# Kernel optimization log

Hardware: AMD Instinct MI355X
Metric: run time of the kernel (lower is better)

Reference implementation:

```python
import math
import jax, jax.numpy as jnp
from jax import lax
import numpy as np

NUM_POINTS = 256      # K sampled points
HIDDEN_DIM = 768
NUM_FREQS = 10
INPUT_DIM = 3 * 2 * NUM_FREQS  # 60


def _fps_indices(pts, k):
    """Furthest point sampling indices for a single cloud pts: [N,3] -> [k] int32.
    Standard iterative FPS starting from index 0."""
    n = pts.shape[0]
    idxs0 = jnp.zeros((k,), dtype=jnp.int32)
    dists0 = jnp.full((n,), jnp.inf, dtype=pts.dtype)

    def body(i, state):
        idxs, dists = state
        last = pts[idxs[i - 1]]                       # [3]
        d = jnp.sum((pts - last) ** 2, axis=-1)       # [N]
        dists = jnp.minimum(dists, d)
        idxs = idxs.at[i].set(jnp.argmax(dists).astype(jnp.int32))
        return (idxs, dists)

    idxs, _ = lax.fori_loop(1, k, body, (idxs0, dists0))
    return idxs


def setup_inputs() -> dict:
    key = jax.random.key(0)
    k1, k2, k3 = jax.random.split(key, 3)
    B, N = 32, 262144
    point_cloud = jax.random.normal(k1, (B, N, 3), dtype=jnp.float32)
    # Xavier-uniform Linear weight [out, in], zero bias (matches _init_weights)
    limit = math.sqrt(6.0 / (INPUT_DIM + HIDDEN_DIM))
    W = jax.random.uniform(k2, (HIDDEN_DIM, INPUT_DIM), jnp.float32, -limit, limit)
    b = jnp.zeros((HIDDEN_DIM,), dtype=jnp.float32)
    return {"point_cloud": point_cloud, "W": W, "b": b}


def reference(point_cloud, W, b):
    B = point_cloud.shape[0]
    # sanitize non-finite (matches torch.where(isfinite, x, 0))
    pc = jnp.where(jnp.isfinite(point_cloud), point_cloud, 0.0)

    # --- furthest point sampling (indices are non-differentiable) ---
    idxs = jax.vmap(lambda p: _fps_indices(lax.stop_gradient(p), NUM_POINTS))(pc)  # [B,K]
    sampled = jnp.take_along_axis(pc, idxs[:, :, None], axis=1)  # [B,K,3]

    # --- per-sample normalization: center then scale by max bbox dim ---
    centroid = jnp.mean(sampled, axis=1, keepdims=True)           # [B,1,3]
    centered = sampled - centroid                                  # [B,K,3]
    bbox = jnp.max(centered, axis=1) - jnp.min(centered, axis=1)   # [B,3]
    max_dim = jnp.max(bbox, axis=-1)                               # [B]
    scale = jnp.where(max_dim > 1e-8, max_dim, 1.0)
    normed = centered / scale[:, None, None]                       # [B,K,3]

    # --- Fourier encoding: sin/cos of coords * 2^f * pi ---
    freqs = jnp.power(2.0, jnp.arange(NUM_FREQS, dtype=jnp.float32))  # [F]
    scaled = normed[..., None] * freqs * jnp.float32(math.pi)         # [B,K,3,F]
    enc = jnp.stack([jnp.sin(scaled), jnp.cos(scaled)], axis=-1)      # [B,K,3,F,2]
    enc = enc.reshape(B, NUM_POINTS, INPUT_DIM)                       # [B,K,60]

    # --- linear projection (torch Linear: x @ W.T + b) ---
    return jnp.einsum('bkd,hd->bkh', enc, W) + b                      # [B,K,768]
```

## Files before the change

### kernel.cpp

```cpp
#include <hip/hip_runtime.h>

#define BATCH 32
#define NPTS  262144
#define KSAMP 256
#define NF    10
#define INDIM 60
#define HID   768

#define NBLK_PER_B 8
#define SLICE (NPTS/NBLK_PER_B)
#define REG_G 4
#define LDS_G 3

#define PI_F 3.14159274101257324f

typedef float v2f __attribute__((ext_vector_type(2)));

__device__ float g_px[BATCH*NPTS];
__device__ float g_py[BATCH*NPTS];
__device__ float g_pz[BATCH*NPTS];
__device__ float g_samp[BATCH*KSAMP*3];
__device__ float g_enc[(size_t)BATCH*KSAMP*INDIM];
__device__ float g_Wt[INDIM*HID];
__device__ unsigned long long g_slot[BATCH][2][NBLK_PER_B];

__device__ __forceinline__ float san(float v){
  float m = v*0.0f;
  return (m == 0.0f) ? v : 0.0f;
}

__global__ __launch_bounds__(256) void region_prepass(const float* __restrict__ pc){
  int bid = blockIdx.x;
  int b   = bid >> 5;
  int rem = bid & 31;
  int q   = rem*1024 + threadIdx.x*4;
  int s   = q >> 12;
  int o   = q & 4095;
  int p   = s*SLICE + 7*4096 + o;
  const float* src = pc + ((size_t)b*NPTS + p)*3;
  float4 A = *(const float4*)(src);
  float4 Bv= *(const float4*)(src+4);
  float4 C = *(const float4*)(src+8);
  float v[12] = {A.x,A.y,A.z,A.w,Bv.x,Bv.y,Bv.z,Bv.w,C.x,C.y,C.z,C.w};
#pragma unroll
  for (int j=0;j<12;j++) v[j] = san(v[j]);
  size_t base = (size_t)b*NPTS + p;
  *(float4*)(g_px+base) = make_float4(v[0],v[3],v[6],v[9]);
  *(float4*)(g_py+base) = make_float4(v[1],v[4],v[7],v[10]);
  *(float4*)(g_pz+base) = make_float4(v[2],v[5],v[8],v[11]);
}

__global__ __launch_bounds__(256) void wtrans(const float* __restrict__ W){
  int idx = blockIdx.x*256 + threadIdx.x;
  int d = idx / HID;
  int h = idx - d*HID;
  g_Wt[idx] = W[h*INDIM + d];
  if (blockIdx.x == 0 && threadIdx.x < 256){
    ((unsigned long long*)g_slot)[threadIdx.x*2+0] = 0ull;
    ((unsigned long long*)g_slot)[threadIdx.x*2+1] = 0ull;
  }
}

__global__ __attribute__((amdgpu_flat_work_group_size(1024,1024)))
           __attribute__((amdgpu_waves_per_eu(4,4)))
void fps_kernel(const float* __restrict__ pc){
#pragma clang fp contract(off)
  __shared__ float4 sX[LDS_G*1024], sY[LDS_G*1024], sZ[LDS_G*1024];
  __shared__ unsigned long long s_cand[2][16];
  __shared__ float s_res[2][4];
  __shared__ int   s_flag[2];

  const int blk = blockIdx.x;
  const int b   = (blk & 7) + 8*(blk >> 6);
  const int s   = (blk >> 3) & 7;
  const int tid = threadIdx.x;
  const int lane = tid & 63, wave = tid >> 6;
  const size_t bN = (size_t)b*NPTS;
  const int soff = s*SLICE;

  v2f rx2[REG_G*2], ry2[REG_G*2], rz2[REG_G*2];
#pragma unroll
  for (int j=0;j<REG_G+LDS_G;j++){
    int p0 = soff + j*4096 + tid*4;
    const float* src = pc + (bN + p0)*3;
    float4 A = *(const float4*)(src);
    float4 Bv= *(const float4*)(src+4);
    float4 C = *(const float4*)(src+8);
    float v[12] = {A.x,A.y,A.z,A.w,Bv.x,Bv.y,Bv.z,Bv.w,C.x,C.y,C.z,C.w};
#pragma unroll
    for (int q=0;q<12;q++) v[q] = san(v[q]);
    if (j < REG_G){
      rx2[j*2+0] = (v2f){v[0], v[3]};  rx2[j*2+1] = (v2f){v[6], v[9]};
      ry2[j*2+0] = (v2f){v[1], v[4]};  ry2[j*2+1] = (v2f){v[7], v[10]};
      rz2[j*2+0] = (v2f){v[2], v[5]};  rz2[j*2+1] = (v2f){v[8], v[11]};
    } else {
      sX[(j-REG_G)*1024+tid] = make_float4(v[0],v[3],v[6],v[9]);
      sY[(j-REG_G)*1024+tid] = make_float4(v[1],v[4],v[7],v[10]);
      sZ[(j-REG_G)*1024+tid] = make_float4(v[2],v[5],v[8],v[11]);
    }
  }

  float d[32];
#pragma unroll
  for (int i=0;i<32;i++) d[i] = __builtin_huge_valf();

  float lx = san(pc[bN*3+0]), ly = san(pc[bN*3+1]), lz = san(pc[bN*3+2]);
  if (s==0 && tid<3) g_samp[(size_t)b*KSAMP*3 + tid] = san(pc[bN*3 + tid]);
  if (tid==0){ s_flag[0]=0; s_flag[1]=0; }
  if (tid<32) s_cand[tid>>4][tid&15] = 0ull;
  __syncthreads();

  const size_t gb = bN + soff + (size_t)7*4096 + tid*4;

  for (int k=1; k<KSAMP; k++){
    const int par = k & 1;
    float4 gx = *(const float4*)(g_px+gb);
    float4 gy = *(const float4*)(g_py+gb);
    float4 gz = *(const float4*)(g_pz+gb);

    v2f l2x = (v2f){lx,lx}, l2y = (v2f){ly,ly}, l2z = (v2f){lz,lz};

    float bestv = -1.0f; int bestc = 0;

#define UPD2(X2,Y2,Z2, DI) { \
      v2f dx_ = (X2) - l2x, dy_ = (Y2) - l2y, dz_ = (Z2) - l2z; \
      v2f dd_ = ((dx_*dx_) + (dy_*dy_)) + (dz_*dz_); \
      float nd0_ = fminf(d[DI], dd_.x);  d[DI] = nd0_; \
      if (nd0_ > bestv){ bestv = nd0_; bestc = (DI); } \
      float nd1_ = fminf(d[(DI)+1], dd_.y);  d[(DI)+1] = nd1_; \
      if (nd1_ > bestv){ bestv = nd1_; bestc = (DI)+1; } }

#pragma unroll
    for (int p=0;p<REG_G*2;p++)
      UPD2(rx2[p], ry2[p], rz2[p], p*2)
#pragma unroll
    for (int j=0;j<LDS_G;j++){
      float4 X = sX[j*1024+tid], Y = sY[j*1024+tid], Z = sZ[j*1024+tid];
      v2f Xa=(v2f){X.x,X.y}, Xb=(v2f){X.z,X.w};
      v2f Ya=(v2f){Y.x,Y.y}, Yb=(v2f){Y.z,Y.w};
      v2f Za=(v2f){Z.x,Z.y}, Zb=(v2f){Z.z,Z.w};
      UPD2(Xa, Ya, Za, (REG_G+j)*4)
      UPD2(Xb, Yb, Zb, (REG_G+j)*4+2)
    }
    {
      v2f Xa=(v2f){gx.x,gx.y}, Xb=(v2f){gx.z,gx.w};
      v2f Ya=(v2f){gy.x,gy.y}, Yb=(v2f){gy.z,gy.w};
      v2f Za=(v2f){gz.x,gz.y}, Zb=(v2f){gz.z,gz.w};
      UPD2(Xa, Ya, Za, 28)
      UPD2(Xb, Yb, Zb, 30)
    }
#undef UPD2

    int besti = soff + ((bestc>>2)<<12) + (tid<<2) + (bestc&3);

#pragma unroll
    for (int off=32; off; off>>=1){
      float ov = __shfl_down(bestv, off);
      int   oi = __shfl_down(besti, off);
      if (ov > bestv || (ov == bestv && oi < besti)){ bestv=ov; besti=oi; }
    }
    unsigned long long wkey = ((unsigned long long)(unsigned)k << 56)
                            | ((unsigned long long)__float_as_uint(bestv) << 24)
                            | (unsigned long long)(0xFFFFFFu ^ (unsigned)besti);
    if (lane==0)
      __hip_atomic_store(&s_cand[par][wave], wkey, __ATOMIC_RELAXED, __HIP_MEMORY_SCOPE_WORKGROUP);

    if (wave==0){
      unsigned long long v;
      for (;;){
        v = __hip_atomic_load(&s_cand[par][lane & 15], __ATOMIC_RELAXED, __HIP_MEMORY_SCOPE_WORKGROUP);
        if ((unsigned)(v >> 56) == (unsigned)k) break;
        __builtin_amdgcn_s_sleep(1);
      }
      __builtin_amdgcn_s_setprio(1);
      unsigned long long pay = v & 0x00FFFFFFFFFFFFFFull;
#pragma unroll
      for (int m=8; m; m>>=1){
        unsigned lo = (unsigned)pay, hi = (unsigned)(pay >> 32);
        unsigned lo2 = __shfl_xor(lo, m), hi2 = __shfl_xor(hi, m);
        unsigned long long o = ((unsigned long long)hi2 << 32) | lo2;
        if (o > pay) pay = o;
      }
      unsigned long long key = ((unsigned long long)(unsigned)k << 56) | pay;
      if (lane==0)
        __hip_atomic_store(&g_slot[b][par][s], key, __ATOMIC_RELAXED, __HIP_MEMORY_SCOPE_AGENT);
      unsigned long long gpay = 0;
      if (lane < NBLK_PER_B){
        unsigned long long gv;
        for (;;){
          gv = __hip_atomic_load(&g_slot[b][par][lane], __ATOMIC_RELAXED, __HIP_MEMORY_SCOPE_AGENT);
          if ((unsigned)(gv >> 56) == (unsigned)k) break;
          __builtin_amdgcn_s_sleep(1);
        }
        gpay = gv & 0x00FFFFFFFFFFFFFFull;
      }
#pragma unroll
      for (int m=4; m; m>>=1){
        unsigned lo = (unsigned)gpay, hi = (unsigned)(gpay >> 32);
        unsigned lo2 = __shfl_xor(lo, m), hi2 = __shfl_xor(hi, m);
        unsigned long long o = ((unsigned long long)hi2 << 32) | lo2;
        if (o > gpay) gpay = o;
      }
      int w = (int)(0xFFFFFFu ^ (unsigned)(gpay & 0xFFFFFFu));
      if (lane < 3){
        float cv = san(pc[(bN + (size_t)w)*3 + lane]);
        s_res[par][lane] = cv;
        if (s==0) g_samp[((size_t)b*KSAMP + k)*3 + lane] = cv;
      }
      if (lane==0)
        __hip_atomic_store(&s_flag[par], k, __ATOMIC_RELEASE, __HIP_MEMORY_SCOPE_WORKGROUP);
      __builtin_amdgcn_s_setprio(0);
      lx = s_res[par][0]; ly = s_res[par][1]; lz = s_res[par][2];
    } else {
      while (__hip_atomic_load(&s_flag[par], __ATOMIC_ACQUIRE, __HIP_MEMORY_SCOPE_WORKGROUP) != k)
        __builtin_amdgcn_s_sleep(1);
      lx = s_res[par][0]; ly = s_res[par][1]; lz = s_res[par][2];
    }
  }
}

template<int OP>
__device__ __forceinline__ float blk_red(float v, float* s4){
  int tid = threadIdx.x;
#pragma unroll
  for (int off=32; off; off>>=1){
    float o = __shfl_down(v, off);
    v = (OP==0) ? v+o : ((OP==1) ? fmaxf(v,o) : fminf(v,o));
  }
  if ((tid&63)==0) s4[tid>>6] = v;
  __syncthreads();
  float r0=s4[0], r1=s4[1], r2=s4[2], r3=s4[3];
  float r = (OP==0) ? ((r0+r1)+(r2+r3))
          : ((OP==1) ? fmaxf(fmaxf(r0,r1),fmaxf(r2,r3))
                     : fminf(fminf(r0,r1),fminf(r2,r3)));
  __syncthreads();
  return r;
}

__global__ __launch_bounds__(256) void norm_encode(){
  __shared__ float s4[4];
  int b = blockIdx.x, k = threadIdx.x;
  const float* sp = &g_samp[((size_t)b*KSAMP + k)*3];
  float x = sp[0], y = sp[1], z = sp[2];

  float cx = blk_red<0>(x, s4) * (1.0f/KSAMP);
  float cy = blk_red<0>(y, s4) * (1.0f/KSAMP);
  float cz = blk_red<0>(z, s4) * (1.0f/KSAMP);

  float ux = __fsub_rn(x,cx), uy = __fsub_rn(y,cy), uz = __fsub_rn(z,cz);

  float mxx = blk_red<1>(ux, s4), mnx = blk_red<2>(ux, s4);
  float mxy = blk_red<1>(uy, s4), mny = blk_red<2>(uy, s4);
  float mxz = blk_red<1>(uz, s4), mnz = blk_red<2>(uz, s4);
  float bx = __fsub_rn(mxx,mnx), by = __fsub_rn(mxy,mny), bz = __fsub_rn(mxz,mnz);
  float md = fmaxf(fmaxf(bx,by),bz);
  float scale = (md > 1e-8f) ? md : 1.0f;

  float n3[3] = { __fdiv_rn(ux,scale), __fdiv_rn(uy,scale), __fdiv_rn(uz,scale) };

  float* e = &g_enc[((size_t)b*KSAMP + k)*INDIM];
#pragma unroll
  for (int c=0;c<3;c++){
    float base = n3[c];
#pragma unroll
    for (int f=0; f<NF; f++){
      float t = __fmul_rn(base, (float)(1<<f));
      float a = __fmul_rn(t, PI_F);
      e[c*2*NF + f*2 + 0] = sinf(a);
      e[c*2*NF + f*2 + 1] = cosf(a);
    }
  }
}

__global__ __launch_bounds__(256) void gemm_kernel(const float* __restrict__ bias,
                                                   float* __restrict__ out){
  __shared__ float s_enc[4*INDIM];
  int blk = blockIdx.x, tid = threadIdx.x;
  int row0 = blk*4;
  if (tid < 4*INDIM) s_enc[tid] = g_enc[(size_t)row0*INDIM + tid];
  __syncthreads();

  float acc[4][3] = {};
  for (int d=0; d<INDIM; d++){
    float w0 = g_Wt[d*HID + tid];
    float w1 = g_Wt[d*HID + tid + 256];
    float w2 = g_Wt[d*HID + tid + 512];
#pragma unroll
    for (int r=0;r<4;r++){
      float ev = s_enc[r*INDIM + d];
      acc[r][0] = fmaf(ev, w0, acc[r][0]);
      acc[r][1] = fmaf(ev, w1, acc[r][1]);
      acc[r][2] = fmaf(ev, w2, acc[r][2]);
    }
  }
  float b0=bias[tid], b1=bias[tid+256], b2=bias[tid+512];
#pragma unroll
  for (int r=0;r<4;r++){
    size_t o = (size_t)(row0+r)*HID;
    out[o+tid]     = acc[r][0]+b0;
    out[o+tid+256] = acc[r][1]+b1;
    out[o+tid+512] = acc[r][2]+b2;
  }
}

extern "C" void kernel_launch(void* const* d_in, const int* in_sizes, int n_in,
                              void* d_out, int out_size, void* d_ws, size_t ws_size,
                              hipStream_t stream){
  const float* pc   = (const float*)d_in[0];
  const float* W    = (const float*)d_in[1];
  const float* bias = (const float*)d_in[2];
  float* out = (float*)d_out;

  region_prepass<<<1024, 256, 0, stream>>>(pc);
  wtrans        <<<(INDIM*HID)/256, 256, 0, stream>>>(W);

  void* args[] = { (void*)&pc };
  hipLaunchCooperativeKernel((void*)fps_kernel, dim3(BATCH*NBLK_PER_B), dim3(1024),
                             args, 0, stream);

  norm_encode<<<BATCH, KSAMP, 0, stream>>>();
  gemm_kernel<<<(BATCH*KSAMP)/4, 256, 0, stream>>>(bias, out);
}
```

Measured before the change: 1.337 ms.

## Carry winner coordinates through FPS reductions so every wave polls global slots directly

```diff
diff --git a/kernel.cpp b/kernel.cpp
--- a/kernel.cpp
+++ b/kernel.cpp
@@ -13,6 +13,7 @@
 #define LDS_G 3
 
 #define PI_F 3.14159274101257324f
+#define PAY56 0x00FFFFFFFFFFFFFFull
 
 typedef float v2f __attribute__((ext_vector_type(2)));
 
@@ -22,11 +23,22 @@
 __device__ float g_samp[BATCH*KSAMP*3];
 __device__ float g_enc[(size_t)BATCH*KSAMP*INDIM];
 __device__ float g_Wt[INDIM*HID];
-__device__ unsigned long long g_slot[BATCH][2][NBLK_PER_B];
+__device__ unsigned long long g_slot[BATCH][2][NBLK_PER_B][3];
 
 __device__ __forceinline__ float san(float v){
   float m = v*0.0f;
   return (m == 0.0f) ? v : 0.0f;
+}
+
+__device__ __forceinline__ unsigned long long shfl64_xor(unsigned long long v, int m){
+  unsigned lo = __shfl_xor((unsigned)v, m);
+  unsigned hi = __shfl_xor((unsigned)(v>>32), m);
+  return ((unsigned long long)hi<<32)|lo;
+}
+__device__ __forceinline__ unsigned long long shfl64(unsigned long long v, int src){
+  unsigned lo = __shfl((unsigned)v, src);
+  unsigned hi = __shfl((unsigned)(v>>32), src);
+  return ((unsigned long long)hi<<32)|lo;
 }
 
 __global__ __launch_bounds__(256) void region_prepass(const float* __restrict__ pc){
@@ -55,9 +67,10 @@
   int d = idx / HID;
   int h = idx - d*HID;
   g_Wt[idx] = W[h*INDIM + d];
-  if (blockIdx.x == 0 && threadIdx.x < 256){
-    ((unsigned long long*)g_slot)[threadIdx.x*2+0] = 0ull;
-    ((unsigned long long*)g_slot)[threadIdx.x*2+1] = 0ull;
+  if (blockIdx.x == 0){
+#pragma unroll
+    for (int r=0;r<6;r++)
+      ((unsigned long long*)g_slot)[threadIdx.x + 256*r] = 0ull;
   }
 }
 
@@ -66,9 +79,7 @@
 void fps_kernel(const float* __restrict__ pc){
 #pragma clang fp contract(off)
   __shared__ float4 sX[LDS_G*1024], sY[LDS_G*1024], sZ[LDS_G*1024];
-  __shared__ unsigned long long s_cand[2][16];
-  __shared__ float s_res[2][4];
-  __shared__ int   s_flag[2];
+  __shared__ unsigned long long s_cand[2][16][3];
 
   const int blk = blockIdx.x;
   const int b   = (blk & 7) + 8*(blk >> 6);
@@ -106,14 +117,14 @@
 
   float lx = san(pc[bN*3+0]), ly = san(pc[bN*3+1]), lz = san(pc[bN*3+2]);
   if (s==0 && tid<3) g_samp[(size_t)b*KSAMP*3 + tid] = san(pc[bN*3 + tid]);
-  if (tid==0){ s_flag[0]=0; s_flag[1]=0; }
-  if (tid<32) s_cand[tid>>4][tid&15] = 0ull;
+  if (tid < 96) ((unsigned long long*)s_cand)[tid] = 0ull;
   __syncthreads();
 
   const size_t gb = bN + soff + (size_t)7*4096 + tid*4;
 
   for (int k=1; k<KSAMP; k++){
     const int par = k & 1;
+    const unsigned long long tagk = (unsigned long long)(unsigned)k << 56;
     float4 gx = *(const float4*)(g_px+gb);
     float4 gy = *(const float4*)(g_py+gb);
     float4 gz = *(const float4*)(g_pz+gb);
@@ -121,14 +132,15 @@
     v2f l2x = (v2f){lx,lx}, l2y = (v2f){ly,ly}, l2z = (v2f){lz,lz};
 
     float bestv = -1.0f; int bestc = 0;
+    float bx = 0.0f, by = 0.0f, bz = 0.0f;
 
 #define UPD2(X2,Y2,Z2, DI) { \
       v2f dx_ = (X2) - l2x, dy_ = (Y2) - l2y, dz_ = (Z2) - l2z; \
       v2f dd_ = ((dx_*dx_) + (dy_*dy_)) + (dz_*dz_); \
       float nd0_ = fminf(d[DI], dd_.x);  d[DI] = nd0_; \
-      if (nd0_ > bestv){ bestv = nd0_; bestc = (DI); } \
+      if (nd0_ > bestv){ bestv = nd0_; bestc = (DI); bx=(X2).x; by=(Y2).x; bz=(Z2).x; } \
       float nd1_ = fminf(d[(DI)+1], dd_.y);  d[(DI)+1] = nd1_; \
-      if (nd1_ > bestv){ bestv = nd1_; bestc = (DI)+1; } }
+      if (nd1_ > bestv){ bestv = nd1_; bestc = (DI)+1; bx=(X2).y; by=(Y2).y; bz=(Z2).y; } }
 
 #pragma unroll
     for (int p=0;p<REG_G*2;p++)
@@ -152,69 +164,96 @@
 #undef UPD2
 
     int besti = soff + ((bestc>>2)<<12) + (tid<<2) + (bestc&3);
-
-#pragma unroll
-    for (int off=32; off; off>>=1){
-      float ov = __shfl_down(bestv, off);
-      int   oi = __shfl_down(besti, off);
-      if (ov > bestv || (ov == bestv && oi < besti)){ bestv=ov; besti=oi; }
-    }
-    unsigned long long wkey = ((unsigned long long)(unsigned)k << 56)
-                            | ((unsigned long long)__float_as_uint(bestv) << 24)
-                            | (unsigned long long)(0xFFFFFFu ^ (unsigned)besti);
-    if (lane==0)
-      __hip_atomic_store(&s_cand[par][wave], wkey, __ATOMIC_RELAXED, __HIP_MEMORY_SCOPE_WORKGROUP);
+    unsigned long long key = ((unsigned long long)__float_as_uint(bestv) << 24)
+                           | (unsigned long long)(0xFFFFFFu ^ (unsigned)besti);
+
+#pragma unroll
+    for (int m=1; m<64; m<<=1){
+      unsigned long long ok = shfl64_xor(key, m);
+      float ox=__shfl_xor(bx,m), oy=__shfl_xor(by,m), oz=__shfl_xor(bz,m);
+      if (ok > key){ key=ok; bx=ox; by=oy; bz=oz; }
+    }
+    if (lane==0){
+      unsigned xb=__float_as_uint(bx), yb=__float_as_uint(by), zb=__float_as_uint(bz);
+      unsigned long long w0 = tagk | key;
+      unsigned long long w1 = tagk | ((unsigned long long)xb<<24) | (yb>>8);
+      unsigned long long w2 = tagk | ((unsigned long long)(yb&0xFFu)<<48)
+                                   | ((unsigned long long)zb<<16);
+      __hip_atomic_store(&s_cand[par][wave][0], w0, __ATOMIC_RELAXED, __HIP_MEMORY_SCOPE_WORKGROUP);
+      __hip_atomic_store(&s_cand[par][wave][1], w1, __ATOMIC_RELAXED, __HIP_MEMORY_SCOPE_WORKGROUP);
+      __hip_atomic_store(&s_cand[par][wave][2], w2, __ATOMIC_RELAXED, __HIP_MEMORY_SCOPE_WORKGROUP);
+    }
 
     if (wave==0){
-      unsigned long long v;
+      unsigned long long pay = 0;
+      if (lane < 48){
+        int wv = lane & 15, word = lane >> 4;
+        unsigned long long v;
+        for (;;){
+          v = __hip_atomic_load(&s_cand[par][wv][word], __ATOMIC_RELAXED, __HIP_MEMORY_SCOPE_WORKGROUP);
+          if ((unsigned)(v >> 56) == (unsigned)k) break;
+          __builtin_amdgcn_s_sleep(1);
+        }
+        pay = v & PAY56;
+      }
+      __builtin_amdgcn_s_setprio(1);
+      unsigned long long bk = pay;
+#pragma unroll
+      for (int m=1; m<16; m<<=1){
+        unsigned long long o = shfl64_xor(bk, m);
+        if (o > bk) bk = o;
+      }
+      unsigned long long wink = shfl64(bk, 0);
+      unsigned long long bal = __ballot(lane<16 && pay==wink);
+      int wv = (int)__ffsll((long long)bal) - 1;
+      unsigned xb =(unsigned)(pay>>24), yh =(unsigned)(pay & 0xFFFFFFu);
+      unsigned yl =(unsigned)((pay>>48)&0xFFu), zb =(unsigned)(pay>>16);
+      unsigned x_b = __shfl(xb, 16+wv);
+      unsigned y_hi= __shfl(yh, 16+wv);
+      unsigned y_lo= __shfl(yl, 32+wv);
+      unsigned z_b = __shfl(zb, 32+wv);
+      unsigned long long w0g = tagk | wink;
+      unsigned long long w1g = tagk | ((unsigned long long)x_b<<24) | y_hi;
+      unsigned long long w2g = tagk | ((unsigned long long)y_lo<<48)
+                                    | ((unsigned long long)z_b<<16);
+      unsigned long long myw = (lane==0) ? w0g : ((lane==1) ? w1g : w2g);
+      if (lane < 3)
+        __hip_atomic_store(&g_slot[b][par][s][lane], myw, __ATOMIC_RELAXED, __HIP_MEMORY_SCOPE_AGENT);
+      __builtin_amdgcn_s_setprio(0);
+    }
+
+    unsigned long long gpay = 0;
+    if (lane < 24){
+      int sl = lane & 7, word = lane >> 3;
+      unsigned long long gv;
       for (;;){
-        v = __hip_atomic_load(&s_cand[par][lane & 15], __ATOMIC_RELAXED, __HIP_MEMORY_SCOPE_WORKGROUP);
-        if ((unsigned)(v >> 56) == (unsigned)k) break;
+        gv = __hip_atomic_load(&g_slot[b][par][sl][word], __ATOMIC_RELAXED, __HIP_MEMORY_SCOPE_AGENT);
+        if ((unsigned)(gv >> 56) == (unsigned)k) break;
         __builtin_amdgcn_s_sleep(1);
       }
-      __builtin_amdgcn_s_setprio(1);
-      unsigned long long pay = v & 0x00FFFFFFFFFFFFFFull;
-#pragma unroll
-      for (int m=8; m; m>>=1){
-        unsigned lo = (unsigned)pay, hi = (unsigned)(pay >> 32);
-        unsigned lo2 = __shfl_xor(lo, m), hi2 = __shfl_xor(hi, m);
-        unsigned long long o = ((unsigned long long)hi2 << 32) | lo2;
-        if (o > pay) pay = o;
-      }
-      unsigned long long key = ((unsigned long long)(unsigned)k << 56) | pay;
-      if (lane==0)
-        __hip_atomic_store(&g_slot[b][par][s], key, __ATOMIC_RELAXED, __HIP_MEMORY_SCOPE_AGENT);
-      unsigned long long gpay = 0;
-      if (lane < NBLK_PER_B){
-        unsigned long long gv;
-        for (;;){
-          gv = __hip_atomic_load(&g_slot[b][par][lane], __ATOMIC_RELAXED, __HIP_MEMORY_SCOPE_AGENT);
-          if ((unsigned)(gv >> 56) == (unsigned)k) break;
-          __builtin_amdgcn_s_sleep(1);
-        }
-        gpay = gv & 0x00FFFFFFFFFFFFFFull;
-      }
-#pragma unroll
-      for (int m=4; m; m>>=1){
-        unsigned lo = (unsigned)gpay, hi = (unsigned)(gpay >> 32);
-        unsigned lo2 = __shfl_xor(lo, m), hi2 = __shfl_xor(hi, m);
-        unsigned long long o = ((unsigned long long)hi2 << 32) | lo2;
-        if (o > gpay) gpay = o;
-      }
-      int w = (int)(0xFFFFFFu ^ (unsigned)(gpay & 0xFFFFFFu));
-      if (lane < 3){
-        float cv = san(pc[(bN + (size_t)w)*3 + lane]);
-        s_res[par][lane] = cv;
-        if (s==0) g_samp[((size_t)b*KSAMP + k)*3 + lane] = cv;
-      }
-      if (lane==0)
-        __hip_atomic_store(&s_flag[par], k, __ATOMIC_RELEASE, __HIP_MEMORY_SCOPE_WORKGROUP);
-      __builtin_amdgcn_s_setprio(0);
-      lx = s_res[par][0]; ly = s_res[par][1]; lz = s_res[par][2];
-    } else {
-      while (__hip_atomic_load(&s_flag[par], __ATOMIC_ACQUIRE, __HIP_MEMORY_SCOPE_WORKGROUP) != k)
-        __builtin_amdgcn_s_sleep(1);
-      lx = s_res[par][0]; ly = s_res[par][1]; lz = s_res[par][2];
+      gpay = gv & PAY56;
+    }
+    unsigned long long gk = gpay;
+#pragma unroll
+    for (int m=1; m<8; m<<=1){
+      unsigned long long o = shfl64_xor(gk, m);
+      if (o > gk) gk = o;
+    }
+    unsigned long long wing = shfl64(gk, 0);
+    unsigned long long gbal = __ballot(lane<8 && gpay==wing);
+    int ws = (int)__ffsll((long long)gbal) - 1;
+    unsigned xb2=(unsigned)(gpay>>24), yh2=(unsigned)(gpay & 0xFFFFFFu);
+    unsigned yl2=(unsigned)((gpay>>48)&0xFFu), zb2=(unsigned)(gpay>>16);
+    unsigned X  = __shfl(xb2,  8+ws);
+    unsigned YH = __shfl(yh2,  8+ws);
+    unsigned YL = __shfl(yl2, 16+ws);
+    unsigned Z  = __shfl(zb2, 16+ws);
+    lx = __uint_as_float(X);
+    ly = __uint_as_float((YH<<8) | YL);
+    lz = __uint_as_float(Z);
+    if (s==0 && wave==0 && lane<3){
+      float cv = (lane==0) ? lx : ((lane==1) ? ly : lz);
+      g_samp[((size_t)b*KSAMP + k)*3 + lane] = cv;
     }
   }
 }
```

Measured after the change: 3.191 ms. +138.6%, slower.

## Replace LDS spin-wait flags in FPS loop with workgroup barriers

Applied to the files above, without the earlier changes.

```diff
diff --git a/kernel.cpp b/kernel.cpp
--- a/kernel.cpp
+++ b/kernel.cpp
@@ -13,6 +13,7 @@
 #define LDS_G 3
 
 #define PI_F 3.14159274101257324f
+#define PAY56 0x00FFFFFFFFFFFFFFull
 
 typedef float v2f __attribute__((ext_vector_type(2)));
 
@@ -27,6 +28,17 @@
 __device__ __forceinline__ float san(float v){
   float m = v*0.0f;
   return (m == 0.0f) ? v : 0.0f;
+}
+
+__device__ __forceinline__ unsigned long long shfl64_xor(unsigned long long v, int m){
+  unsigned lo = __shfl_xor((unsigned)v, m);
+  unsigned hi = __shfl_xor((unsigned)(v>>32), m);
+  return ((unsigned long long)hi<<32)|lo;
+}
+__device__ __forceinline__ unsigned long long shfl64(unsigned long long v, int src){
+  unsigned lo = __shfl((unsigned)v, src);
+  unsigned hi = __shfl((unsigned)(v>>32), src);
+  return ((unsigned long long)hi<<32)|lo;
 }
 
 __global__ __launch_bounds__(256) void region_prepass(const float* __restrict__ pc){
@@ -66,9 +78,8 @@
 void fps_kernel(const float* __restrict__ pc){
 #pragma clang fp contract(off)
   __shared__ float4 sX[LDS_G*1024], sY[LDS_G*1024], sZ[LDS_G*1024];
-  __shared__ unsigned long long s_cand[2][16];
-  __shared__ float s_res[2][4];
-  __shared__ int   s_flag[2];
+  __shared__ unsigned long long s_cand[16];
+  __shared__ float s_res[4];
 
   const int blk = blockIdx.x;
   const int b   = (blk & 7) + 8*(blk >> 6);
@@ -106,14 +117,13 @@
 
   float lx = san(pc[bN*3+0]), ly = san(pc[bN*3+1]), lz = san(pc[bN*3+2]);
   if (s==0 && tid<3) g_samp[(size_t)b*KSAMP*3 + tid] = san(pc[bN*3 + tid]);
-  if (tid==0){ s_flag[0]=0; s_flag[1]=0; }
-  if (tid<32) s_cand[tid>>4][tid&15] = 0ull;
   __syncthreads();
 
   const size_t gb = bN + soff + (size_t)7*4096 + tid*4;
 
   for (int k=1; k<KSAMP; k++){
     const int par = k & 1;
+    const unsigned long long tagk = (unsigned long long)(unsigned)k << 56;
     float4 gx = *(const float4*)(g_px+gb);
     float4 gy = *(const float4*)(g_py+gb);
     float4 gz = *(const float4*)(g_pz+gb);
@@ -159,63 +169,49 @@
       int   oi = __shfl_down(besti, off);
       if (ov > bestv || (ov == bestv && oi < besti)){ bestv=ov; besti=oi; }
     }
-    unsigned long long wkey = ((unsigned long long)(unsigned)k << 56)
-                            | ((unsigned long long)__float_as_uint(bestv) << 24)
-                            | (unsigned long long)(0xFFFFFFu ^ (unsigned)besti);
     if (lane==0)
-      __hip_atomic_store(&s_cand[par][wave], wkey, __ATOMIC_RELAXED, __HIP_MEMORY_SCOPE_WORKGROUP);
+      s_cand[wave] = ((unsigned long long)__float_as_uint(bestv) << 24)
+                   | (unsigned long long)(0xFFFFFFu ^ (unsigned)besti);
+
+    __syncthreads();
 
     if (wave==0){
-      unsigned long long v;
-      for (;;){
-        v = __hip_atomic_load(&s_cand[par][lane & 15], __ATOMIC_RELAXED, __HIP_MEMORY_SCOPE_WORKGROUP);
-        if ((unsigned)(v >> 56) == (unsigned)k) break;
-        __builtin_amdgcn_s_sleep(1);
-      }
-      __builtin_amdgcn_s_setprio(1);
-      unsigned long long pay = v & 0x00FFFFFFFFFFFFFFull;
-#pragma unroll
-      for (int m=8; m; m>>=1){
-        unsigned lo = (unsigned)pay, hi = (unsigned)(pay >> 32);
-        unsigned lo2 = __shfl_xor(lo, m), hi2 = __shfl_xor(hi, m);
-        unsigned long long o = ((unsigned long long)hi2 << 32) | lo2;
+      unsigned long long pay = (lane < 16) ? s_cand[lane] : 0ull;
+#pragma unroll
+      for (int m=1; m<16; m<<=1){
+        unsigned long long o = shfl64_xor(pay, m);
         if (o > pay) pay = o;
       }
-      unsigned long long key = ((unsigned long long)(unsigned)k << 56) | pay;
       if (lane==0)
-        __hip_atomic_store(&g_slot[b][par][s], key, __ATOMIC_RELAXED, __HIP_MEMORY_SCOPE_AGENT);
+        __hip_atomic_store(&g_slot[b][par][s], tagk | pay,
+                           __ATOMIC_RELAXED, __HIP_MEMORY_SCOPE_AGENT);
       unsigned long long gpay = 0;
       if (lane < NBLK_PER_B){
         unsigned long long gv;
         for (;;){
-          gv = __hip_atomic_load(&g_slot[b][par][lane], __ATOMIC_RELAXED, __HIP_MEMORY_SCOPE_AGENT);
+          gv = __hip_atomic_load(&g_slot[b][par][lane],
+                                 __ATOMIC_RELAXED, __HIP_MEMORY_SCOPE_AGENT);
           if ((unsigned)(gv >> 56) == (unsigned)k) break;
-          __builtin_amdgcn_s_sleep(1);
         }
-        gpay = gv & 0x00FFFFFFFFFFFFFFull;
+        gpay = gv & PAY56;
       }
 #pragma unroll
-      for (int m=4; m; m>>=1){
-        unsigned lo = (unsigned)gpay, hi = (unsigned)(gpay >> 32);
-        unsigned lo2 = __shfl_xor(lo, m), hi2 = __shfl_xor(hi, m);
-        unsigned long long o = ((unsigned long long)hi2 << 32) | lo2;
+      for (int m=1; m<8; m<<=1){
+        unsigned long long o = shfl64_xor(gpay, m);
         if (o > gpay) gpay = o;
       }
-      int w = (int)(0xFFFFFFu ^ (unsigned)(gpay & 0xFFFFFFu));
+      unsigned long long wing = shfl64(gpay, 0);
+      unsigned w = 0xFFFFFFu ^ (unsigned)(wing & 0xFFFFFFu);
+      int wu = __builtin_amdgcn_readfirstlane((int)w);
       if (lane < 3){
-        float cv = san(pc[(bN + (size_t)w)*3 + lane]);
-        s_res[par][lane] = cv;
+        float cv = san(pc[(bN + (size_t)(unsigned)wu)*3 + lane]);
+        s_res[lane] = cv;
         if (s==0) g_samp[((size_t)b*KSAMP + k)*3 + lane] = cv;
       }
-      if (lane==0)
-        __hip_atomic_store(&s_flag[par], k, __ATOMIC_RELEASE, __HIP_MEMORY_SCOPE_WORKGROUP);
-      __builtin_amdgcn_s_setprio(0);
-      lx = s_res[par][0]; ly = s_res[par][1]; lz = s_res[par][2];
-    } else {
-      while (__hip_atomic_load(&s_flag[par], __ATOMIC_ACQUIRE, __HIP_MEMORY_SCOPE_WORKGROUP) != k)
-        __builtin_amdgcn_s_sleep(1);
-      lx = s_res[par][0]; ly = s_res[par][1]; lz = s_res[par][2];
-    }
+    }
+
+    __syncthreads();
+    lx = s_res[0]; ly = s_res[1]; lz = s_res[2];
   }
 }
 
```

Result: no change. 1.330 ms (-0.5%).
